# Kernel tuning notes

Measured on AMD Instinct MI355X. Metric: run time of the kernel, lower is better.

## Reference

```python
import jax, jax.numpy as jnp
import numpy as np

MARGIN = 0.3


def setup_inputs() -> dict:
    key = jax.random.key(0)
    k1, k2 = jax.random.split(key)
    B, D = 4096, 1024
    z_anchor = jax.random.normal(k1, (B, D), dtype=jnp.float32)
    z_positive = jax.random.normal(k2, (B, D), dtype=jnp.float32)
    return {"z_anchor": z_anchor, "z_positive": z_positive}


def reference(z_anchor, z_positive):
    B = z_anchor.shape[0]
    a = z_anchor / jnp.linalg.norm(z_anchor, axis=1, keepdims=True)
    p = z_positive / jnp.linalg.norm(z_positive, axis=1, keepdims=True)

    pos_dist = 1.0 - jnp.sum(a * p, axis=1)                 # [B]
    neg_dist_mat = 1.0 - jnp.einsum('bd,cd->bc', a, p)      # [B,B]

    offdiag = ~jnp.eye(B, dtype=bool)
    pd = pos_dist[:, None]
    semi_hard = offdiag & (neg_dist_mat > pd) & (neg_dist_mat < pd + MARGIN)

    cnt = jnp.sum(semi_hard, axis=1)                        # [B]
    mean_semi = jnp.sum(jnp.where(semi_hard, neg_dist_mat, 0.0), axis=1) / jnp.maximum(cnt, 1)
    min_offdiag = jnp.min(jnp.where(offdiag, neg_dist_mat, jnp.inf), axis=1)

    neg_dist = jnp.where(cnt > 0, mean_semi, min_offdiag)   # [B]
    loss = jnp.mean(jax.nn.relu(pos_dist - neg_dist + MARGIN))
    return loss
```

## Files before the change

kernel.cpp:

```cpp
#include <hip/hip_runtime.h>
#include <stdint.h>

#define MARGIN 0.3f

typedef __bf16 bf16x8_t __attribute__((ext_vector_type(8)));
typedef float f32x4_t __attribute__((ext_vector_type(4)));

static constexpr int NB = 4096;
static constexpr int ND = 1024;
static constexpr int BM = 128;
static constexpr int BN = 128;
static constexpr int BK = 64;

__device__ __forceinline__ unsigned short f2bf(float x) {
  union { float f; unsigned u; } v; v.f = x;
  unsigned r = v.u + 0x7FFFu + ((v.u >> 16) & 1u);
  return (unsigned short)(r >> 16);
}

__device__ __forceinline__ void gload_lds16(const void* g, void* l) {
  __builtin_amdgcn_global_load_lds(
      reinterpret_cast<const __attribute__((address_space(1))) uint32_t*>(
          reinterpret_cast<uintptr_t>(g)),
      reinterpret_cast<__attribute__((address_space(3))) uint32_t*>(
          reinterpret_cast<uintptr_t>(l)),
      16, 0, 0);
}

__global__ __launch_bounds__(256) void norm_kernel(
    const float* __restrict__ za, const float* __restrict__ zp,
    __bf16* __restrict__ Ah, __bf16* __restrict__ Ph,
    float* __restrict__ pos, float* __restrict__ ssum,
    int* __restrict__ scnt, unsigned* __restrict__ smin) {
  const int b = blockIdx.x;
  const int t = threadIdx.x;
  const float4 av = reinterpret_cast<const float4*>(za + (size_t)b * ND)[t];
  const float4 pv = reinterpret_cast<const float4*>(zp + (size_t)b * ND)[t];
  float sa = av.x * av.x + av.y * av.y + av.z * av.z + av.w * av.w;
  float sp = pv.x * pv.x + pv.y * pv.y + pv.z * pv.z + pv.w * pv.w;
  float dp = av.x * pv.x + av.y * pv.y + av.z * pv.z + av.w * pv.w;
#pragma unroll
  for (int off = 1; off < 64; off <<= 1) {
    sa += __shfl_xor(sa, off);
    sp += __shfl_xor(sp, off);
    dp += __shfl_xor(dp, off);
  }
  __shared__ float red[3][4];
  const int wid = t >> 6, lane = t & 63;
  if (lane == 0) { red[0][wid] = sa; red[1][wid] = sp; red[2][wid] = dp; }
  __syncthreads();
  sa = red[0][0] + red[0][1] + red[0][2] + red[0][3];
  sp = red[1][0] + red[1][1] + red[1][2] + red[1][3];
  dp = red[2][0] + red[2][1] + red[2][2] + red[2][3];
  const float rsa = rsqrtf(sa), rsp = rsqrtf(sp);
  if (t == 0) {
    pos[b] = 1.0f - dp * rsa * rsp;
    ssum[b] = 0.0f;
    scnt[b] = 0;
    smin[b] = 0x7F800000u;
  }
  ushort4 oa, op;
  oa.x = f2bf(av.x * rsa); oa.y = f2bf(av.y * rsa);
  oa.z = f2bf(av.z * rsa); oa.w = f2bf(av.w * rsa);
  op.x = f2bf(pv.x * rsp); op.y = f2bf(pv.y * rsp);
  op.z = f2bf(pv.z * rsp); op.w = f2bf(pv.w * rsp);
  reinterpret_cast<ushort4*>(reinterpret_cast<unsigned short*>(Ah) + (size_t)b * ND)[t] = oa;
  reinterpret_cast<ushort4*>(reinterpret_cast<unsigned short*>(Ph) + (size_t)b * ND)[t] = op;
}

__global__ __launch_bounds__(256) void gemm_stats_kernel(
    const __bf16* __restrict__ Ah, const __bf16* __restrict__ Ph,
    const float* __restrict__ pos, float* __restrict__ ssum,
    int* __restrict__ scnt, unsigned* __restrict__ smin) {
  __shared__ __align__(16) __bf16 As[BM * BK];
  __shared__ __align__(16) __bf16 Bs[BN * BK];
  const int t = threadIdx.x;
  const int lane = t & 63;
  const int wid = t >> 6;
  const int wr = wid >> 1, wc = wid & 1;
  const int g = lane >> 4, c = lane & 15;
  const int row0 = blockIdx.y * BM;
  const int col0 = blockIdx.x * BN;

  f32x4_t acc[4][4] = {};

  const int sr = t >> 3;
  const int sk = (t & 7) * 8;
  const __bf16* Ag = Ah + (size_t)(row0 + sr) * ND + sk;
  const __bf16* Bg = Ph + (size_t)(col0 + sr) * ND + sk;

  for (int kt = 0; kt < ND / BK; ++kt) {
    __syncthreads();
    const __bf16* Agk = Ag + kt * BK;
    const __bf16* Bgk = Bg + kt * BK;
#pragma unroll
    for (int i = 0; i < 4; ++i) {
      gload_lds16(Agk + (size_t)i * 32 * ND, As + i * 2048 + wid * 512);
      gload_lds16(Bgk + (size_t)i * 32 * ND, Bs + i * 2048 + wid * 512);
    }
    __syncthreads();
#pragma unroll
    for (int kk = 0; kk < 2; ++kk) {
      bf16x8_t af[4], bfv[4];
#pragma unroll
      for (int m = 0; m < 4; ++m)
        af[m] = *reinterpret_cast<const bf16x8_t*>(
            As + (wr * 64 + m * 16 + c) * BK + kk * 32 + g * 8);
#pragma unroll
      for (int n = 0; n < 4; ++n)
        bfv[n] = *reinterpret_cast<const bf16x8_t*>(
            Bs + (wc * 64 + n * 16 + c) * BK + kk * 32 + g * 8);
#pragma unroll
      for (int m = 0; m < 4; ++m)
#pragma unroll
        for (int n = 0; n < 4; ++n)
          acc[m][n] = __builtin_amdgcn_mfma_f32_16x16x32_bf16(
              af[m], bfv[n], acc[m][n], 0, 0, 0);
    }
  }

#pragma unroll
  for (int m = 0; m < 4; ++m) {
#pragma unroll
    for (int r = 0; r < 4; ++r) {
      const int grow = row0 + wr * 64 + m * 16 + g * 4 + r;
      const float pd = pos[grow];
      float s = 0.0f;
      int ct = 0;
      float mn = 3.0e38f;
#pragma unroll
      for (int n = 0; n < 4; ++n) {
        const int gcol = col0 + wc * 64 + n * 16 + c;
        const float v = 1.0f - acc[m][n][r];
        if (gcol != grow) {
          mn = fminf(mn, v);
          if (v > pd && v < pd + MARGIN) { s += v; ct += 1; }
        }
      }
#pragma unroll
      for (int off = 1; off < 16; off <<= 1) {
        s += __shfl_xor(s, off);
        ct += __shfl_xor(ct, off);
        mn = fminf(mn, __shfl_xor(mn, off));
      }
      if (c == 0) {
        atomicAdd(&ssum[grow], s);
        atomicAdd(&scnt[grow], ct);
        atomicMin(&smin[grow], __float_as_uint(mn));
      }
    }
  }
}

__global__ __launch_bounds__(256) void finalize_kernel(
    const float* __restrict__ pos, const float* __restrict__ ssum,
    const int* __restrict__ scnt, const unsigned* __restrict__ smin,
    float* __restrict__ out) {
  const int t = threadIdx.x;
  float acc = 0.0f;
  for (int rr = t; rr < NB; rr += 256) {
    const float pd = pos[rr];
    const int ct = scnt[rr];
    const float neg = ct > 0 ? ssum[rr] / (float)ct : __uint_as_float(smin[rr]);
    acc += fmaxf(pd - neg + MARGIN, 0.0f);
  }
#pragma unroll
  for (int off = 1; off < 64; off <<= 1) acc += __shfl_xor(acc, off);
  __shared__ float red[4];
  if ((t & 63) == 0) red[t >> 6] = acc;
  __syncthreads();
  if (t == 0) out[0] = (red[0] + red[1] + red[2] + red[3]) * (1.0f / NB);
}

extern "C" void kernel_launch(void* const* d_in, const int* in_sizes, int n_in,
                              void* d_out, int out_size, void* d_ws, size_t ws_size,
                              hipStream_t stream) {
  const float* za = (const float*)d_in[0];
  const float* zp = (const float*)d_in[1];
  float* out = (float*)d_out;
  char* ws = (char*)d_ws;
  __bf16* Ah = (__bf16*)(ws);
  __bf16* Ph = (__bf16*)(ws + (size_t)NB * ND * 2);
  float* pos = (float*)(ws + (size_t)NB * ND * 4);
  float* ssum = pos + NB;
  int* scnt = (int*)(ssum + NB);
  unsigned* smin = (unsigned*)(scnt + NB);

  norm_kernel<<<NB, 256, 0, stream>>>(za, zp, Ah, Ph, pos, ssum, scnt, smin);
  gemm_stats_kernel<<<dim3(NB / BN, NB / BM), 256, 0, stream>>>(
      Ah, Ph, pos, ssum, scnt, smin);
  finalize_kernel<<<1, 256, 0, stream>>>(pos, ssum, scnt, smin, out);
}
```

Baseline: 156.9 us.

## Rewrite GEMM as 256x256 tile, 8-wave, double-buffered pipelined kernel with swizzled LDS

Replaces the 128x128 single-buffered GEMM with a 256x256-tile, 512-thread kernel. It uses 128KB of dynamic LDS, double-buffered global-to-LDS staging, XOR-swizzled LDS addressing to avoid bank conflicts, and fine-grained barriers that interleave loads with MFMA quarters under raised wave priority. Workgroup IDs are remapped for L2 locality. The goal is to hide load latency behind compute and raise arithmetic intensity per tile, at the cost of 256 workgroups for 256 CUs and a large register footprint.

```diff
diff --git a/kernel.cpp b/kernel.cpp
--- a/kernel.cpp
+++ b/kernel.cpp
@@ -8,9 +8,8 @@
 
 static constexpr int NB = 4096;
 static constexpr int ND = 1024;
-static constexpr int BM = 128;
-static constexpr int BN = 128;
-static constexpr int BK = 64;
+static constexpr int NKT = ND / 64;
+static constexpr int NIT = NKT / 2;
 
 __device__ __forceinline__ unsigned short f2bf(float x) {
   union { float f; unsigned u; } v; v.f = x;
@@ -68,62 +67,115 @@
   reinterpret_cast<ushort4*>(reinterpret_cast<unsigned short*>(Ph) + (size_t)b * ND)[t] = op;
 }
 
-__global__ __launch_bounds__(256) void gemm_stats_kernel(
+
+#define BAR   __builtin_amdgcn_s_barrier()
+#define LGKM0 asm volatile("s_waitcnt lgkmcnt(0)" ::: "memory")
+#define VM4   asm volatile("s_waitcnt vmcnt(4)" ::: "memory")
+#define VM0   asm volatile("s_waitcnt vmcnt(0)" ::: "memory")
+#define PRIO1 __builtin_amdgcn_s_setprio(1)
+#define PRIO0 __builtin_amdgcn_s_setprio(0)
+
+#define STAGE_A(buf, half, kt) do { \
+    const char* _g = (const char*)Ah + (size_t)(row0 + (half)*128 + srow) * 2048 + (size_t)(kt)*128 + scolb; \
+    char* _l = smem + (buf)*32768 + (half)*16384 + w*1024; \
+    gload_lds16(_g, _l); \
+    gload_lds16(_g + 64*2048, _l + 8192); \
+  } while (0)
+
+#define STAGE_B(buf, half, kt) do { \
+    const char* _g = (const char*)Ph + (size_t)(col0 + (half)*128 + srow) * 2048 + (size_t)(kt)*128 + scolb; \
+    char* _l = smem + 65536 + (buf)*32768 + (half)*16384 + w*1024; \
+    gload_lds16(_g, _l); \
+    gload_lds16(_g + 64*2048, _l + 8192); \
+  } while (0)
+
+#define LD_A(buf, mh) do { _Pragma("unroll") \
+    for (int mm = 0; mm < 4; ++mm) { \
+      const char* _p = smem + (buf)*32768 + (wr*128 + (mh)*64 + mm*16 + c) * 128; \
+      aq[mm][0] = *(const bf16x8_t*)(_p + cswz0); \
+      aq[mm][1] = *(const bf16x8_t*)(_p + cswz1); \
+    } } while (0)
+
+#define LD_B(buf, nh, dst) do { _Pragma("unroll") \
+    for (int nn = 0; nn < 2; ++nn) { \
+      const char* _p = smem + 65536 + (buf)*32768 + (wc*64 + (nh)*32 + nn*16 + c) * 128; \
+      dst[nn][0] = *(const bf16x8_t*)(_p + cswz0); \
+      dst[nn][1] = *(const bf16x8_t*)(_p + cswz1); \
+    } } while (0)
+
+#define MFMA_Q(mh, bq, nh) do { _Pragma("unroll") \
+    for (int kk = 0; kk < 2; ++kk) { _Pragma("unroll") \
+      for (int mm = 0; mm < 4; ++mm) { _Pragma("unroll") \
+        for (int nn = 0; nn < 2; ++nn) \
+          acc[(mh)*4+mm][(nh)*2+nn] = __builtin_amdgcn_mfma_f32_16x16x32_bf16( \
+              aq[mm][kk], bq[nn][kk], acc[(mh)*4+mm][(nh)*2+nn], 0, 0, 0); \
+      } } } while (0)
+
+__global__ __launch_bounds__(512, 2) void gemm8_kernel(
     const __bf16* __restrict__ Ah, const __bf16* __restrict__ Ph,
     const float* __restrict__ pos, float* __restrict__ ssum,
     int* __restrict__ scnt, unsigned* __restrict__ smin) {
-  __shared__ __align__(16) __bf16 As[BM * BK];
-  __shared__ __align__(16) __bf16 Bs[BN * BK];
+  extern __shared__ char smem[];
   const int t = threadIdx.x;
   const int lane = t & 63;
-  const int wid = t >> 6;
-  const int wr = wid >> 1, wc = wid & 1;
-  const int g = lane >> 4, c = lane & 15;
-  const int row0 = blockIdx.y * BM;
-  const int col0 = blockIdx.x * BN;
-
-  f32x4_t acc[4][4] = {};
-
-  const int sr = t >> 3;
-  const int sk = (t & 7) * 8;
-  const __bf16* Ag = Ah + (size_t)(row0 + sr) * ND + sk;
-  const __bf16* Bg = Ph + (size_t)(col0 + sr) * ND + sk;
-
-  for (int kt = 0; kt < ND / BK; ++kt) {
-    __syncthreads();
-    const __bf16* Agk = Ag + kt * BK;
-    const __bf16* Bgk = Bg + kt * BK;
-#pragma unroll
-    for (int i = 0; i < 4; ++i) {
-      gload_lds16(Agk + (size_t)i * 32 * ND, As + i * 2048 + wid * 512);
-      gload_lds16(Bgk + (size_t)i * 32 * ND, Bs + i * 2048 + wid * 512);
-    }
-    __syncthreads();
-#pragma unroll
-    for (int kk = 0; kk < 2; ++kk) {
-      bf16x8_t af[4], bfv[4];
-#pragma unroll
-      for (int m = 0; m < 4; ++m)
-        af[m] = *reinterpret_cast<const bf16x8_t*>(
-            As + (wr * 64 + m * 16 + c) * BK + kk * 32 + g * 8);
-#pragma unroll
-      for (int n = 0; n < 4; ++n)
-        bfv[n] = *reinterpret_cast<const bf16x8_t*>(
-            Bs + (wc * 64 + n * 16 + c) * BK + kk * 32 + g * 8);
-#pragma unroll
-      for (int m = 0; m < 4; ++m)
-#pragma unroll
-        for (int n = 0; n < 4; ++n)
-          acc[m][n] = __builtin_amdgcn_mfma_f32_16x16x32_bf16(
-              af[m], bfv[n], acc[m][n], 0, 0, 0);
-    }
-  }
-
-#pragma unroll
-  for (int m = 0; m < 4; ++m) {
+  const int w = t >> 6;
+  const int wr = w >> 2, wc = w & 3;
+  const int c = lane & 15, g = lane >> 4;
+
+  const int wg = blockIdx.x;
+  const int swzid = (wg & 7) * 32 + (wg >> 3);
+  const int by = swzid >> 4, bx = swzid & 15;
+  const int row0 = by * 256, col0 = bx * 256;
+
+  const int srow = w * 8 + (lane >> 3);
+  const int scolb = ((lane & 7) << 4) ^ (((lane >> 3) & 7) << 4);
+  const int cswz0 = (g * 16) ^ ((c & 7) << 4);
+  const int cswz1 = (64 + g * 16) ^ ((c & 7) << 4);
+
+  f32x4_t acc[8][4] = {};
+  bf16x8_t aq[4][2], bq0[2][2], bq1[2][2];
+
+  STAGE_B(0, 0, 0); STAGE_B(0, 1, 0);
+  STAGE_A(0, 0, 0); STAGE_A(0, 1, 0);
+  STAGE_B(1, 0, 1); STAGE_B(1, 1, 1);
+  VM4; BAR;
+
+  for (int i = 0; i < NIT; ++i) {
+    const int o = 2 * i + 1;
+    const bool st = (i < NIT - 1);
+    LD_A(0, 0); LD_B(0, 0, bq0);
+    STAGE_A(1, 0, o);
+    BAR; LGKM0; PRIO1; MFMA_Q(0, bq0, 0); PRIO0; BAR;
+    LD_B(0, 1, bq1);
+    STAGE_A(1, 1, o);
+    BAR; LGKM0; PRIO1; MFMA_Q(0, bq1, 1); PRIO0; BAR;
+    LD_A(0, 1);
+    if (st) STAGE_B(0, 0, o + 1);
+    BAR; LGKM0; PRIO1; MFMA_Q(1, bq0, 0); PRIO0; BAR;
+    if (st) STAGE_B(0, 1, o + 1);
+    PRIO1; MFMA_Q(1, bq1, 1); PRIO0;
+    if (st) { VM4; } else { VM0; }
+    BAR;
+    LD_A(1, 0); LD_B(1, 0, bq0);
+    if (st) STAGE_A(0, 0, o + 1);
+    BAR; LGKM0; PRIO1; MFMA_Q(0, bq0, 0); PRIO0; BAR;
+    LD_B(1, 1, bq1);
+    if (st) STAGE_A(0, 1, o + 1);
+    BAR; LGKM0; PRIO1; MFMA_Q(0, bq1, 1); PRIO0; BAR;
+    LD_A(1, 1);
+    if (st) STAGE_B(1, 0, o + 2);
+    BAR; LGKM0; PRIO1; MFMA_Q(1, bq0, 0); PRIO0; BAR;
+    if (st) STAGE_B(1, 1, o + 2);
+    PRIO1; MFMA_Q(1, bq1, 1); PRIO0;
+    if (st) { VM4; } else { VM0; }
+    BAR;
+  }
+
+#pragma unroll
+  for (int m = 0; m < 8; ++m) {
 #pragma unroll
     for (int r = 0; r < 4; ++r) {
-      const int grow = row0 + wr * 64 + m * 16 + g * 4 + r;
+      const int grow = row0 + wr * 128 + m * 16 + g * 4 + r;
       const float pd = pos[grow];
       float s = 0.0f;
       int ct = 0;
@@ -157,17 +209,19 @@
     const int* __restrict__ scnt, const unsigned* __restrict__ smin,
     float* __restrict__ out) {
   const int t = threadIdx.x;
-  float acc = 0.0f;
-  for (int rr = t; rr < NB; rr += 256) {
+  float accv = 0.0f;
+#pragma unroll
+  for (int it = 0; it < NB / 256; ++it) {
+    const int rr = t + it * 256;
     const float pd = pos[rr];
     const int ct = scnt[rr];
     const float neg = ct > 0 ? ssum[rr] / (float)ct : __uint_as_float(smin[rr]);
-    acc += fmaxf(pd - neg + MARGIN, 0.0f);
-  }
-#pragma unroll
-  for (int off = 1; off < 64; off <<= 1) acc += __shfl_xor(acc, off);
+    accv += fmaxf(pd - neg + MARGIN, 0.0f);
+  }
+#pragma unroll
+  for (int off = 1; off < 64; off <<= 1) accv += __shfl_xor(accv, off);
   __shared__ float red[4];
-  if ((t & 63) == 0) red[t >> 6] = acc;
+  if ((t & 63) == 0) red[t >> 6] = accv;
   __syncthreads();
   if (t == 0) out[0] = (red[0] + red[1] + red[2] + red[3]) * (1.0f / NB);
 }
@@ -186,8 +240,10 @@
   int* scnt = (int*)(ssum + NB);
   unsigned* smin = (unsigned*)(scnt + NB);
 
+  (void)hipFuncSetAttribute((const void*)gemm8_kernel,
+                            hipFuncAttributeMaxDynamicSharedMemorySize, 131072);
+
   norm_kernel<<<NB, 256, 0, stream>>>(za, zp, Ah, Ph, pos, ssum, scnt, smin);
-  gemm_stats_kernel<<<dim3(NB / BN, NB / BM), 256, 0, stream>>>(
-      Ah, Ph, pos, ssum, scnt, smin);
+  gemm8_kernel<<<256, 512, 131072, stream>>>(Ah, Ph, pos, ssum, scnt, smin);
   finalize_kernel<<<1, 256, 0, stream>>>(pos, ssum, scnt, smin, out);
 }
```

Measured after the change: 133.8 us. 14.7% less time.
